# Kernel tuning notes

Hardware: AMD Instinct MI355X
Metric: run time of the kernel (lower is better)

Reference implementation:

```python
import jax, jax.numpy as jnp
import numpy as np
import math

NUM_HEADS = 8
RES_K = 9  # res_kernel_size


def setup_inputs() -> dict:
    key = jax.random.key(0)
    ks = jax.random.split(key, 6)
    N, C, h, w = 8, 256, 64, 64
    x = jax.random.normal(ks[0], (N, C, h, w), dtype=jnp.float32)
    w_qkv = jax.random.normal(ks[1], (3 * C, C), dtype=jnp.float32) * 0.02
    b_qkv = jax.random.normal(ks[2], (3 * C,), dtype=jnp.float32) * 0.02
    w_proj = jax.random.normal(ks[3], (C, C), dtype=jnp.float32) * 0.02
    b_proj = jax.random.normal(ks[4], (C,), dtype=jnp.float32) * 0.02
    w_dconv = jax.random.normal(ks[5], (NUM_HEADS, 1, RES_K, 1), dtype=jnp.float32) * 0.1
    return {"x": x, "w_qkv": w_qkv, "b_qkv": b_qkv,
            "w_proj": w_proj, "b_proj": b_proj, "w_dconv": w_dconv}


def _l2norm(t):
    # torch x / x.norm(dim=-1, keepdim=True): plain L2 norm, no eps
    return t / jnp.linalg.norm(t, axis=-1, keepdims=True)


def reference(x, w_qkv, b_qkv, w_proj, b_proj, w_dconv):
    N, C, h, w = x.shape
    H = NUM_HEADS
    D = C // H
    L = h * w
    xt = x.reshape(N, C, L).transpose(0, 2, 1)  # [N, L, C]
    qkv = xt @ w_qkv.T + b_qkv                   # [N, L, 3C]
    qkv = qkv.reshape(N, L, 3, H, D).transpose(2, 0, 3, 1, 4)  # [3, N, H, L, D]
    q, k, v = qkv[0], qkv[1], qkv[2]
    q = _l2norm(q)
    k = _l2norm(k)
    # depthwise conv over token dim: v as NCHW with C=H, H=L, W=D
    pad = RES_K // 2
    dconv_v = jax.lax.conv_general_dilated(
        v, w_dconv, window_strides=(1, 1), padding=[(pad, pad), (0, 0)],
        dimension_numbers=("NCHW", "OIHW", "NCHW"), feature_group_count=H)
    attn = jnp.einsum("nhld,nhle->nhde", k, v)   # [N, H, D, D]
    out = 0.5 * v + (1.0 / math.pi) * jnp.einsum("nhld,nhde->nhle", q, attn)
    out = _l2norm(out)
    out = out + dconv_v
    out = out.transpose(0, 2, 1, 3).reshape(N, L, C)  # [N, L, C]
    out = out @ w_proj.T + b_proj
    return out.transpose(0, 2, 1).reshape(N, C, h, w)
```

## Files before the change

kernel.cpp:

```cpp
#include <hip/hip_runtime.h>

#define NB 8
#define CC 256
#define HH 8
#define DD 32
#define LL 4096

typedef short v8s __attribute__((ext_vector_type(8)));
typedef float v4f __attribute__((ext_vector_type(4)));
typedef unsigned short v8u __attribute__((ext_vector_type(8)));
typedef unsigned short v4us __attribute__((ext_vector_type(4)));

__device__ __forceinline__ float4 ld4(const float* p) { return *(const float4*)p; }

__device__ __forceinline__ unsigned short f2bf(float f) {
    union { float f; unsigned int u; } v; v.f = f;
    unsigned int r = (v.u + 0x7FFFu + ((v.u >> 16) & 1u)) >> 16;
    return (unsigned short)r;
}
__device__ __forceinline__ float bf2f(unsigned short u) {
    union { unsigned int u; float f; } v; v.u = ((unsigned int)u) << 16;
    return v.f;
}

__device__ __forceinline__ void gl_lds16(const unsigned short* g, unsigned short* l) {
    __builtin_amdgcn_global_load_lds(
        (const __attribute__((address_space(1))) void*)g,
        (__attribute__((address_space(3))) void*)l, 16, 0, 0);
}

__global__ __launch_bounds__(256) void cvt2_k(
    const float* __restrict__ a, const float* __restrict__ b,
    unsigned short* __restrict__ da, unsigned short* __restrict__ db,
    float* __restrict__ attn)
{
    int i = blockIdx.x * 256 + threadIdx.x;
    if (i < 3 * CC * CC) da[i] = f2bf(a[i]);
    else if (i < 4 * CC * CC) db[i - 3 * CC * CC] = f2bf(b[i - 3 * CC * CC]);
    else attn[i - 4 * CC * CC] = 0.f;
}

#define PADC 264
__global__ __launch_bounds__(256) void transpose_x_k(
    const float* __restrict__ x, unsigned short* __restrict__ xb)
{
    __shared__ unsigned short t[32][PADC];
    const int n = blockIdx.y;
    const int l0 = blockIdx.x * 32;
    const float* xn = x + (size_t)n * CC * LL;
    const int lam = threadIdx.x & 31;
    const int cb = threadIdx.x >> 5;
#pragma unroll
    for (int i = 0; i < 32; ++i) {
        int c = cb * 32 + i;
        t[lam][c] = f2bf(xn[(size_t)c * LL + l0 + lam]);
    }
    __syncthreads();
    unsigned short* dst = xb + ((size_t)n * LL + l0) * CC;
    const int tid = threadIdx.x;
#pragma unroll
    for (int i = 0; i < 4; ++i) {
        int f = i * 2048 + tid * 8;
        int lr = f >> 8;
        int c2 = f & 255;
        v8u val = *(const v8u*)&t[lr][c2];
        *(v8u*)(dst + f) = val;
    }
}

__global__ __launch_bounds__(256, 2) void gemm_qkv_mfma(
    const unsigned short* __restrict__ xb, const unsigned short* __restrict__ wqb,
    const float* __restrict__ bqkv,
    unsigned short* __restrict__ q, unsigned short* __restrict__ k,
    unsigned short* __restrict__ v)
{
    __shared__ __align__(16) unsigned short xs[8192];
    __shared__ __align__(16) unsigned short wsb[16384];

    const int bid  = blockIdx.x;
    const int xcd  = bid & 7;
    const int slot = bid >> 3;
    const int jt   = slot % 3;
    const int p    = slot / 3;
    const int gp   = xcd * 32 + p;
    const int l0   = (gp & 31) * 128;
    const int n    = gp >> 5;
    const int j0   = jt * 256;

    const int tid = threadIdx.x;
    const int lane = tid & 63, wave = tid >> 6;
    const int wr = wave >> 1, wc = wave & 1;
    const int r = lane & 15, quad = lane >> 4;

    const int srow = wave * 8 + (lane >> 3);
    const int dchunk = (lane & 7) ^ (lane >> 3);
    const unsigned short* xg = xb + (size_t)n * LL * CC
                             + (size_t)(l0 + srow) * CC + dchunk * 8;
    const unsigned short* wg = wqb + (size_t)(j0 + srow) * CC + dchunk * 8;
    unsigned short* xls = xs + wave * 512 + lane * 8;
    unsigned short* wls = wsb + wave * 512 + lane * 8;

    v4f acc[8][4];
#pragma unroll
    for (int mi = 0; mi < 8; ++mi)
#pragma unroll
        for (int nj = 0; nj < 4; ++nj) acc[mi][nj] = (v4f)(0.f);

    const int jbase = wr * 128;
    const int lbase = wc * 64;

    for (int kt = 0; kt < 4; ++kt) {
        if (kt) __syncthreads();
        const int c0 = kt * 64;
#pragma unroll
        for (int i = 0; i < 4; ++i)
            gl_lds16(xg + (size_t)i * 32 * CC + c0, xls + i * 2048);
#pragma unroll
        for (int i = 0; i < 8; ++i)
            gl_lds16(wg + (size_t)i * 32 * CC + c0, wls + i * 2048);
        __syncthreads();

#pragma unroll
        for (int kk = 0; kk < 2; ++kk) {
            const int cfrag = kk * 4 + quad;
            const int s = cfrag ^ (r & 7);
            v8s b[4];
#pragma unroll
            for (int nj = 0; nj < 4; ++nj) {
                int lloc = lbase + nj * 16 + r;
                b[nj] = *(const v8s*)(xs + lloc * 64 + s * 8);
            }
            v8s a[8];
#pragma unroll
            for (int mi = 0; mi < 8; ++mi) {
                int jloc = jbase + mi * 16 + r;
                a[mi] = *(const v8s*)(wsb + jloc * 64 + s * 8);
            }
#pragma unroll
            for (int mi = 0; mi < 8; ++mi)
#pragma unroll
                for (int nj = 0; nj < 4; ++nj)
                    acc[mi][nj] = __builtin_amdgcn_mfma_f32_16x16x32_bf16(
                        a[mi], b[nj], acc[mi][nj], 0, 0, 0);
        }
    }

    unsigned short* base = (jt == 0 ? q : (jt == 1 ? k : v));

    float bias[8][4];
#pragma unroll
    for (int mi = 0; mi < 8; ++mi)
        *(float4*)bias[mi] = *(const float4*)(bqkv + j0 + jbase + mi * 16 + quad * 4);

    unsigned short* dstp[8];
#pragma unroll
    for (int mi = 0; mi < 8; ++mi) {
        int hh = wr * 4 + (mi >> 1);
        int d0 = (mi & 1) * 16 + quad * 4;
        dstp[mi] = base + (size_t)(n * HH + hh) * LL * DD + d0;
    }

    if (jt < 2) {
#pragma unroll
        for (int nj = 0; nj < 4; ++nj) {
            float t[8][4];
            float ss[4] = {0.f, 0.f, 0.f, 0.f};
#pragma unroll
            for (int mi = 0; mi < 8; ++mi)
#pragma unroll
                for (int reg = 0; reg < 4; ++reg) {
                    float val = acc[mi][nj][reg] + bias[mi][reg];
                    t[mi][reg] = val;
                    ss[mi >> 1] += val * val;
                }
#pragma unroll
            for (int h4 = 0; h4 < 4; ++h4) {
                ss[h4] += __shfl_xor(ss[h4], 16);
                ss[h4] += __shfl_xor(ss[h4], 32);
                ss[h4] = rsqrtf(ss[h4]);
            }
            size_t l = (size_t)(l0 + lbase + nj * 16 + r);
#pragma unroll
            for (int mi = 0; mi < 8; ++mi) {
                float rn = ss[mi >> 1];
                v4us pk;
#pragma unroll
                for (int reg = 0; reg < 4; ++reg) pk[reg] = f2bf(t[mi][reg] * rn);
                *(v4us*)(dstp[mi] + l * DD) = pk;
            }
        }
    } else {
#pragma unroll
        for (int nj = 0; nj < 4; ++nj) {
            size_t l = (size_t)(l0 + lbase + nj * 16 + r);
#pragma unroll
            for (int mi = 0; mi < 8; ++mi) {
                v4us pk;
#pragma unroll
                for (int reg = 0; reg < 4; ++reg)
                    pk[reg] = f2bf(acc[mi][nj][reg] + bias[mi][reg]);
                *(v4us*)(dstp[mi] + l * DD) = pk;
            }
        }
    }
}

__global__ __launch_bounds__(256) void attn_k(
    const unsigned short* __restrict__ k, const unsigned short* __restrict__ v,
    float* __restrict__ attn)
{
    __shared__ float red[4][1024];
    const int nh = blockIdx.y;
    const int wv = threadIdx.x >> 6;
    const int lane = threadIdx.x & 63;
    const int eg = lane & 7;
    const int dg = lane >> 3;
    const int l0 = blockIdx.x * 512 + wv * 128;
    const unsigned short* kb = k + (size_t)nh * LL * DD;
    const unsigned short* vb = v + (size_t)nh * LL * DD;
    float acc[4][4] = {};
#pragma unroll 4
    for (int l = l0; l < l0 + 128; ++l) {
        v4us k4 = *(const v4us*)(kb + (size_t)l * DD + dg * 4);
        v4us v4 = *(const v4us*)(vb + (size_t)l * DD + eg * 4);
        float ka[4] = {bf2f(k4[0]), bf2f(k4[1]), bf2f(k4[2]), bf2f(k4[3])};
        float va[4] = {bf2f(v4[0]), bf2f(v4[1]), bf2f(v4[2]), bf2f(v4[3])};
#pragma unroll
        for (int dp = 0; dp < 4; ++dp)
#pragma unroll
            for (int ep = 0; ep < 4; ++ep)
                acc[dp][ep] += ka[dp] * va[ep];
    }
#pragma unroll
    for (int dp = 0; dp < 4; ++dp)
#pragma unroll
        for (int ep = 0; ep < 4; ++ep)
            red[wv][(dg * 4 + dp) * 32 + eg * 4 + ep] = acc[dp][ep];
    __syncthreads();
    float* ap = attn + (size_t)nh * 1024;
    for (int i = threadIdx.x; i < 1024; i += 256)
        atomicAdd(&ap[i], red[0][i] + red[1][i] + red[2][i] + red[3][i]);
}

#define TOK 256
__global__ __launch_bounds__(256) void mid_k(
    const unsigned short* __restrict__ q, const unsigned short* __restrict__ v,
    const float* __restrict__ attn, const float* __restrict__ wd,
    unsigned short* __restrict__ midb)
{
    __shared__ float vt[TOK + 8][34];
    const int nh = blockIdx.y;
    const int n = nh >> 3, hh = nh & 7;
    const int l0 = blockIdx.x * TOK;
    const int tid = threadIdx.x;
    const int lane = tid & 63, wave = tid >> 6;
    const int r = lane & 15, quad = lane >> 4;
    const unsigned short* vb = v + (size_t)nh * LL * DD;

    for (int f = tid; f < (TOK + 8) * 4; f += 256) {
        int row = f >> 2, seg = f & 3;
        int l = l0 - 4 + row;
        float tmp[8];
        if (l >= 0 && l < LL) {
            v8u v8 = *(const v8u*)(vb + (size_t)l * DD + seg * 8);
#pragma unroll
            for (int j = 0; j < 8; ++j) tmp[j] = bf2f(v8[j]);
        } else {
#pragma unroll
            for (int j = 0; j < 8; ++j) tmp[j] = 0.f;
        }
#pragma unroll
        for (int j = 0; j < 8; ++j) vt[row][seg * 8 + j] = tmp[j];
    }

    v8s bfrag[2];
#pragma unroll
    for (int et = 0; et < 2; ++et) {
        int e = et * 16 + r;
#pragma unroll
        for (int j = 0; j < 8; ++j)
            ((unsigned short*)&bfrag[et])[j] =
                f2bf(attn[(size_t)nh * 1024 + (quad * 8 + j) * 32 + e]);
    }

    float wc[9];
#pragma unroll
    for (int r9 = 0; r9 < 9; ++r9) wc[r9] = wd[hh * 9 + r9];

    __syncthreads();

    const unsigned short* qb = q + (size_t)nh * LL * DD;
    unsigned short* ob = midb + (size_t)n * LL * CC + hh * DD;

#pragma unroll
    for (int tp = 0; tp < 4; ++tp) {
        const int tb = wave * 64 + tp * 16;
        v8s afrag = *(const v8s*)(qb + (size_t)(l0 + tb + r) * DD + quad * 8);
        v4f acc[2] = {(v4f)(0.f), (v4f)(0.f)};
#pragma unroll
        for (int et = 0; et < 2; ++et)
            acc[et] = __builtin_amdgcn_mfma_f32_16x16x32_bf16(afrag, bfrag[et], acc[et], 0, 0, 0);

        float vcol[2][12];
#pragma unroll
        for (int et = 0; et < 2; ++et) {
            int e = et * 16 + r;
#pragma unroll
            for (int o = 0; o < 12; ++o)
                vcol[et][o] = vt[tb + quad * 4 + o][e];
        }

        float t[2][4], ss[4];
#pragma unroll
        for (int reg = 0; reg < 4; ++reg) {
            t[0][reg] = 0.5f * vcol[0][4 + reg] + 0.31830988618379067f * acc[0][reg];
            t[1][reg] = 0.5f * vcol[1][4 + reg] + 0.31830988618379067f * acc[1][reg];
            ss[reg] = t[0][reg] * t[0][reg] + t[1][reg] * t[1][reg];
        }
#pragma unroll
        for (int m = 1; m < 16; m <<= 1)
#pragma unroll
            for (int reg = 0; reg < 4; ++reg)
                ss[reg] += __shfl_xor(ss[reg], m);
#pragma unroll
        for (int reg = 0; reg < 4; ++reg) ss[reg] = rsqrtf(ss[reg]);

#pragma unroll
        for (int et = 0; et < 2; ++et) {
            int e = et * 16 + r;
#pragma unroll
            for (int reg = 0; reg < 4; ++reg) {
                float dv = 0.f;
#pragma unroll
                for (int r9 = 0; r9 < 9; ++r9) dv += wc[r9] * vcol[et][reg + r9];
                int l = l0 + tb + quad * 4 + reg;
                ob[(size_t)l * CC + e] = f2bf(t[et][reg] * ss[reg] + dv);
            }
        }
    }
}

__global__ __launch_bounds__(256, 2) void gemm_proj_mfma(
    const unsigned short* __restrict__ midb, const unsigned short* __restrict__ wpb,
    const float* __restrict__ bp, float* __restrict__ out)
{
    __shared__ __align__(16) unsigned short xs[8192];
    __shared__ __align__(16) unsigned short wsb[8192];

    const int bid  = blockIdx.x;
    const int xcd  = bid & 7;
    const int slot = bid >> 3;
    const int jt   = slot & 1;
    const int p    = slot >> 1;
    const int gp   = xcd * 32 + p;
    const int l0   = (gp & 31) * 128;
    const int n    = gp >> 5;
    const int j0   = jt * 128;

    const int tid = threadIdx.x;
    const int lane = tid & 63, wave = tid >> 6;
    const int wr = wave >> 1, wc = wave & 1;
    const int r = lane & 15, quad = lane >> 4;

    const int srow = wave * 8 + (lane >> 3);
    const int dchunk = (lane & 7) ^ (lane >> 3);
    const unsigned short* xg = midb + (size_t)n * LL * CC
                             + (size_t)(l0 + srow) * CC + dchunk * 8;
    const unsigned short* wg = wpb + (size_t)(j0 + srow) * CC + dchunk * 8;
    unsigned short* xls = xs + wave * 512 + lane * 8;
    unsigned short* wls = wsb + wave * 512 + lane * 8;

    v4f acc[4][4];
#pragma unroll
    for (int mi = 0; mi < 4; ++mi)
#pragma unroll
        for (int nj = 0; nj < 4; ++nj) acc[mi][nj] = (v4f)(0.f);

    const int jbase = wr * 64;
    const int lbase = wc * 64;

    for (int kt = 0; kt < 4; ++kt) {
        if (kt) __syncthreads();
        const int c0 = kt * 64;
#pragma unroll
        for (int i = 0; i < 4; ++i) {
            gl_lds16(xg + (size_t)i * 32 * CC + c0, xls + i * 2048);
            gl_lds16(wg + (size_t)i * 32 * CC + c0, wls + i * 2048);
        }
        __syncthreads();

        v8s a[4][2], b[4][2];
#pragma unroll
        for (int kk = 0; kk < 2; ++kk) {
            const int cfrag = kk * 4 + quad;
#pragma unroll
            for (int mi = 0; mi < 4; ++mi) {
                int jloc = jbase + mi * 16 + r;
                int s = cfrag ^ (r & 7);
                a[mi][kk] = *(const v8s*)(wsb + jloc * 64 + s * 8);
            }
#pragma unroll
            for (int nj = 0; nj < 4; ++nj) {
                int lloc = lbase + nj * 16 + r;
                int s = cfrag ^ (r & 7);
                b[nj][kk] = *(const v8s*)(xs + lloc * 64 + s * 8);
            }
        }
#pragma unroll
        for (int kk = 0; kk < 2; ++kk)
#pragma unroll
            for (int mi = 0; mi < 4; ++mi)
#pragma unroll
                for (int nj = 0; nj < 4; ++nj)
                    acc[mi][nj] = __builtin_amdgcn_mfma_f32_16x16x32_bf16(
                        a[mi][kk], b[nj][kk], acc[mi][nj], 0, 0, 0);
    }

#pragma unroll
    for (int mi = 0; mi < 4; ++mi)
#pragma unroll
        for (int reg = 0; reg < 4; ++reg) {
            int j = j0 + jbase + mi * 16 + quad * 4 + reg;
            float bias = bp[j];
#pragma unroll
            for (int nj = 0; nj < 4; ++nj) {
                int l = l0 + lbase + nj * 16 + r;
                out[((size_t)n * CC + j) * LL + l] = acc[mi][nj][reg] + bias;
            }
        }
}

extern "C" void kernel_launch(void* const* d_in, const int* in_sizes, int n_in,
                              void* d_out, int out_size, void* d_ws, size_t ws_size,
                              hipStream_t stream)
{
    const float* x     = (const float*)d_in[0];
    const float* wqkv  = (const float*)d_in[1];
    const float* bqkv  = (const float*)d_in[2];
    const float* wproj = (const float*)d_in[3];
    const float* bproj = (const float*)d_in[4];
    const float* wd    = (const float*)d_in[5];
    float* out = (float*)d_out;

    const size_t QKV = (size_t)NB * HH * LL * DD;
    unsigned short* q = (unsigned short*)d_ws;
    unsigned short* k = q + QKV;
    unsigned short* v = k + QKV;
    float* attn = (float*)(v + QKV);
    unsigned short* xb = (unsigned short*)(attn + (size_t)NB * HH * DD * DD);
    unsigned short* midb = xb;
    unsigned short* wqb = xb + (size_t)NB * LL * CC;
    unsigned short* wpb = wqb + 3 * CC * CC;

    cvt2_k<<<1280, 256, 0, stream>>>(wqkv, wproj, wqb, wpb, attn);
    transpose_x_k<<<dim3(128, 8), 256, 0, stream>>>(x, xb);
    gemm_qkv_mfma<<<768, 256, 0, stream>>>(xb, wqb, bqkv, q, k, v);
    attn_k<<<dim3(8, 64), 256, 0, stream>>>(k, v, attn);
    mid_k<<<dim3(LL / TOK, 64), 256, 0, stream>>>(q, v, attn, wd, midb);
    gemm_proj_mfma<<<512, 256, 0, stream>>>(midb, wpb, bproj, out);
}
```

Before: 157.8 us.

## Fuse mid stage into projection GEMM and merge prep kernels

The per-head mid computation (q·attn, normalisation, depthwise conv) now writes its bf16 result into a swizzled shared-memory tile, and the same block runs the output projection GEMM on it. This avoids the round trip of the intermediate tensor through global memory and one kernel launch. The weight conversion, attn zeroing and x transpose are merged into a single vectorised prep kernel. In exchange, each block computes all 8 heads for 64 tokens and reads the projection weights directly from global memory/L2 without LDS staging, which may cost bandwidth and occupancy.

```diff
diff --git a/kernel.cpp b/kernel.cpp
--- a/kernel.cpp
+++ b/kernel.cpp
@@ -29,42 +29,57 @@
         (__attribute__((address_space(3))) void*)l, 16, 0, 0);
 }
 
-__global__ __launch_bounds__(256) void cvt2_k(
-    const float* __restrict__ a, const float* __restrict__ b,
-    unsigned short* __restrict__ da, unsigned short* __restrict__ db,
+#define PADC 264
+__global__ __launch_bounds__(256) void prep_k(
+    const float* __restrict__ x, unsigned short* __restrict__ xb,
+    const float* __restrict__ wq, const float* __restrict__ wp,
+    unsigned short* __restrict__ dwq, unsigned short* __restrict__ dwp,
     float* __restrict__ attn)
 {
-    int i = blockIdx.x * 256 + threadIdx.x;
-    if (i < 3 * CC * CC) da[i] = f2bf(a[i]);
-    else if (i < 4 * CC * CC) db[i - 3 * CC * CC] = f2bf(b[i - 3 * CC * CC]);
-    else attn[i - 4 * CC * CC] = 0.f;
-}
-
-#define PADC 264
-__global__ __launch_bounds__(256) void transpose_x_k(
-    const float* __restrict__ x, unsigned short* __restrict__ xb)
-{
     __shared__ unsigned short t[32][PADC];
-    const int n = blockIdx.y;
-    const int l0 = blockIdx.x * 32;
-    const float* xn = x + (size_t)n * CC * LL;
-    const int lam = threadIdx.x & 31;
-    const int cb = threadIdx.x >> 5;
-#pragma unroll
-    for (int i = 0; i < 32; ++i) {
-        int c = cb * 32 + i;
-        t[lam][c] = f2bf(xn[(size_t)c * LL + l0 + lam]);
-    }
-    __syncthreads();
-    unsigned short* dst = xb + ((size_t)n * LL + l0) * CC;
-    const int tid = threadIdx.x;
-#pragma unroll
-    for (int i = 0; i < 4; ++i) {
-        int f = i * 2048 + tid * 8;
-        int lr = f >> 8;
-        int c2 = f & 255;
-        v8u val = *(const v8u*)&t[lr][c2];
-        *(v8u*)(dst + f) = val;
+    const int bid = blockIdx.x;
+    if (bid < 1024) {
+        const int n = bid >> 7;
+        const int l0 = (bid & 127) * 32;
+        const float* xn = x + (size_t)n * CC * LL;
+        const int lam = threadIdx.x & 31;
+        const int cb = threadIdx.x >> 5;
+#pragma unroll
+        for (int i = 0; i < 32; ++i) {
+            int c = cb * 32 + i;
+            t[lam][c] = f2bf(xn[(size_t)c * LL + l0 + lam]);
+        }
+        __syncthreads();
+        unsigned short* dst = xb + ((size_t)n * LL + l0) * CC;
+        const int tid = threadIdx.x;
+#pragma unroll
+        for (int i = 0; i < 4; ++i) {
+            int f = i * 2048 + tid * 8;
+            int lr = f >> 8;
+            int c2 = f & 255;
+            v8u val = *(const v8u*)&t[lr][c2];
+            *(v8u*)(dst + f) = val;
+        }
+    } else {
+        int ti = (bid - 1024) * 256 + threadIdx.x;
+        if (ti < 24576) {
+            int i = ti * 8;
+            float4 f0 = ld4(wq + i), f1 = ld4(wq + i + 4);
+            v8u o;
+            o[0] = f2bf(f0.x); o[1] = f2bf(f0.y); o[2] = f2bf(f0.z); o[3] = f2bf(f0.w);
+            o[4] = f2bf(f1.x); o[5] = f2bf(f1.y); o[6] = f2bf(f1.z); o[7] = f2bf(f1.w);
+            *(v8u*)(dwq + i) = o;
+        } else if (ti < 32768) {
+            int i = (ti - 24576) * 8;
+            float4 f0 = ld4(wp + i), f1 = ld4(wp + i + 4);
+            v8u o;
+            o[0] = f2bf(f0.x); o[1] = f2bf(f0.y); o[2] = f2bf(f0.z); o[3] = f2bf(f0.w);
+            o[4] = f2bf(f1.x); o[5] = f2bf(f1.y); o[6] = f2bf(f1.z); o[7] = f2bf(f1.w);
+            *(v8u*)(dwp + i) = o;
+        } else {
+            int i = (ti - 32768) * 4;
+            *(float4*)(attn + i) = make_float4(0.f, 0.f, 0.f, 0.f);
+        }
     }
 }
 
@@ -242,168 +257,139 @@
         atomicAdd(&ap[i], red[0][i] + red[1][i] + red[2][i] + red[3][i]);
 }
 
-#define TOK 256
-__global__ __launch_bounds__(256) void mid_k(
+#define PTOK 64
+#define VTP 40
+__global__ __launch_bounds__(256, 2) void midproj_k(
     const unsigned short* __restrict__ q, const unsigned short* __restrict__ v,
     const float* __restrict__ attn, const float* __restrict__ wd,
-    unsigned short* __restrict__ midb)
+    const unsigned short* __restrict__ wpb, const float* __restrict__ bp,
+    float* __restrict__ out)
 {
-    __shared__ float vt[TOK + 8][34];
-    const int nh = blockIdx.y;
-    const int n = nh >> 3, hh = nh & 7;
-    const int l0 = blockIdx.x * TOK;
+    __shared__ __align__(16) unsigned short vt[8 * 72 * VTP];
+    __shared__ __align__(16) unsigned short smid[4 * 64 * 64];
+
+    const int n  = blockIdx.y;
+    const int l0 = blockIdx.x * PTOK;
     const int tid = threadIdx.x;
     const int lane = tid & 63, wave = tid >> 6;
     const int r = lane & 15, quad = lane >> 4;
-    const unsigned short* vb = v + (size_t)nh * LL * DD;
-
-    for (int f = tid; f < (TOK + 8) * 4; f += 256) {
-        int row = f >> 2, seg = f & 3;
+
+    const unsigned short* vbase = v + (size_t)(n * HH) * LL * DD;
+#pragma unroll
+    for (int it = 0; it < 9; ++it) {
+        int task = it * 256 + tid;
+        int seg = task & 3;
+        int hr = task >> 2;
+        int row = hr % 72;
+        int h = hr / 72;
         int l = l0 - 4 + row;
-        float tmp[8];
-        if (l >= 0 && l < LL) {
-            v8u v8 = *(const v8u*)(vb + (size_t)l * DD + seg * 8);
-#pragma unroll
-            for (int j = 0; j < 8; ++j) tmp[j] = bf2f(v8[j]);
-        } else {
-#pragma unroll
-            for (int j = 0; j < 8; ++j) tmp[j] = 0.f;
-        }
-#pragma unroll
-        for (int j = 0; j < 8; ++j) vt[row][seg * 8 + j] = tmp[j];
-    }
-
-    v8s bfrag[2];
-#pragma unroll
-    for (int et = 0; et < 2; ++et) {
-        int e = et * 16 + r;
-#pragma unroll
-        for (int j = 0; j < 8; ++j)
-            ((unsigned short*)&bfrag[et])[j] =
-                f2bf(attn[(size_t)nh * 1024 + (quad * 8 + j) * 32 + e]);
-    }
-
-    float wc[9];
-#pragma unroll
-    for (int r9 = 0; r9 < 9; ++r9) wc[r9] = wd[hh * 9 + r9];
-
+        v8u val;
+        if (l >= 0 && l < LL)
+            val = *(const v8u*)(vbase + ((size_t)h * LL + l) * DD + seg * 8);
+        else
+            val = (v8u)(unsigned short)0;
+        *(v8u*)(&vt[hr * VTP + seg * 8]) = val;
+    }
     __syncthreads();
 
-    const unsigned short* qb = q + (size_t)nh * LL * DD;
-    unsigned short* ob = midb + (size_t)n * LL * CC + hh * DD;
-
-#pragma unroll
-    for (int tp = 0; tp < 4; ++tp) {
-        const int tb = wave * 64 + tp * 16;
-        v8s afrag = *(const v8s*)(qb + (size_t)(l0 + tb + r) * DD + quad * 8);
-        v4f acc[2] = {(v4f)(0.f), (v4f)(0.f)};
-#pragma unroll
-        for (int et = 0; et < 2; ++et)
-            acc[et] = __builtin_amdgcn_mfma_f32_16x16x32_bf16(afrag, bfrag[et], acc[et], 0, 0, 0);
-
-        float vcol[2][12];
+    const float inv_pi = 0.31830988618379067f;
+#pragma unroll
+    for (int hi = 0; hi < 2; ++hi) {
+        const int h = wave * 2 + hi;
+        const int nh = n * HH + h;
+        const unsigned short* qb = q + (size_t)nh * LL * DD;
+        const unsigned short* vth = vt + h * 72 * VTP;
+
+        v8s bfrag[2];
 #pragma unroll
         for (int et = 0; et < 2; ++et) {
             int e = et * 16 + r;
 #pragma unroll
-            for (int o = 0; o < 12; ++o)
-                vcol[et][o] = vt[tb + quad * 4 + o][e];
-        }
-
-        float t[2][4], ss[4];
-#pragma unroll
-        for (int reg = 0; reg < 4; ++reg) {
-            t[0][reg] = 0.5f * vcol[0][4 + reg] + 0.31830988618379067f * acc[0][reg];
-            t[1][reg] = 0.5f * vcol[1][4 + reg] + 0.31830988618379067f * acc[1][reg];
-            ss[reg] = t[0][reg] * t[0][reg] + t[1][reg] * t[1][reg];
-        }
-#pragma unroll
-        for (int m = 1; m < 16; m <<= 1)
-#pragma unroll
-            for (int reg = 0; reg < 4; ++reg)
-                ss[reg] += __shfl_xor(ss[reg], m);
-#pragma unroll
-        for (int reg = 0; reg < 4; ++reg) ss[reg] = rsqrtf(ss[reg]);
-
-#pragma unroll
-        for (int et = 0; et < 2; ++et) {
-            int e = et * 16 + r;
+            for (int j = 0; j < 8; ++j)
+                ((unsigned short*)&bfrag[et])[j] =
+                    f2bf(attn[(size_t)nh * 1024 + (quad * 8 + j) * 32 + e]);
+        }
+        float wc[9];
+#pragma unroll
+        for (int r9 = 0; r9 < 9; ++r9) wc[r9] = wd[h * 9 + r9];
+
+#pragma unroll
+        for (int lt = 0; lt < 4; ++lt) {
+            const int tb = lt * 16;
+            v8s afrag = *(const v8s*)(qb + (size_t)(l0 + tb + r) * DD + quad * 8);
+            v4f acc[2] = {(v4f)(0.f), (v4f)(0.f)};
+#pragma unroll
+            for (int et = 0; et < 2; ++et)
+                acc[et] = __builtin_amdgcn_mfma_f32_16x16x32_bf16(
+                    afrag, bfrag[et], acc[et], 0, 0, 0);
+
+            float vcol[2][12];
+#pragma unroll
+            for (int et = 0; et < 2; ++et) {
+                int e = et * 16 + r;
+#pragma unroll
+                for (int o = 0; o < 12; ++o)
+                    vcol[et][o] = bf2f(vth[(tb + quad * 4 + o) * VTP + e]);
+            }
+
+            float t[2][4], ss[4];
 #pragma unroll
             for (int reg = 0; reg < 4; ++reg) {
-                float dv = 0.f;
-#pragma unroll
-                for (int r9 = 0; r9 < 9; ++r9) dv += wc[r9] * vcol[et][reg + r9];
-                int l = l0 + tb + quad * 4 + reg;
-                ob[(size_t)l * CC + e] = f2bf(t[et][reg] * ss[reg] + dv);
-            }
-        }
-    }
-}
-
-__global__ __launch_bounds__(256, 2) void gemm_proj_mfma(
-    const unsigned short* __restrict__ midb, const unsigned short* __restrict__ wpb,
-    const float* __restrict__ bp, float* __restrict__ out)
-{
-    __shared__ __align__(16) unsigned short xs[8192];
-    __shared__ __align__(16) unsigned short wsb[8192];
-
-    const int bid  = blockIdx.x;
-    const int xcd  = bid & 7;
-    const int slot = bid >> 3;
-    const int jt   = slot & 1;
-    const int p    = slot >> 1;
-    const int gp   = xcd * 32 + p;
-    const int l0   = (gp & 31) * 128;
-    const int n    = gp >> 5;
-    const int j0   = jt * 128;
-
-    const int tid = threadIdx.x;
-    const int lane = tid & 63, wave = tid >> 6;
-    const int wr = wave >> 1, wc = wave & 1;
-    const int r = lane & 15, quad = lane >> 4;
-
-    const int srow = wave * 8 + (lane >> 3);
-    const int dchunk = (lane & 7) ^ (lane >> 3);
-    const unsigned short* xg = midb + (size_t)n * LL * CC
-                             + (size_t)(l0 + srow) * CC + dchunk * 8;
-    const unsigned short* wg = wpb + (size_t)(j0 + srow) * CC + dchunk * 8;
-    unsigned short* xls = xs + wave * 512 + lane * 8;
-    unsigned short* wls = wsb + wave * 512 + lane * 8;
-
+                t[0][reg] = 0.5f * vcol[0][4 + reg] + inv_pi * acc[0][reg];
+                t[1][reg] = 0.5f * vcol[1][4 + reg] + inv_pi * acc[1][reg];
+                ss[reg] = t[0][reg] * t[0][reg] + t[1][reg] * t[1][reg];
+            }
+#pragma unroll
+            for (int m = 1; m < 16; m <<= 1)
+#pragma unroll
+                for (int reg = 0; reg < 4; ++reg)
+                    ss[reg] += __shfl_xor(ss[reg], m);
+#pragma unroll
+            for (int reg = 0; reg < 4; ++reg) ss[reg] = rsqrtf(ss[reg]);
+
+#pragma unroll
+            for (int et = 0; et < 2; ++et) {
+                int c = h * 32 + et * 16 + r;
+                int chunk = c >> 6, c6 = c & 63;
+                int goff = c6 & 7;
+#pragma unroll
+                for (int reg = 0; reg < 4; ++reg) {
+                    float dv = 0.f;
+#pragma unroll
+                    for (int r9 = 0; r9 < 9; ++r9) dv += wc[r9] * vcol[et][reg + r9];
+                    int l = tb + quad * 4 + reg;
+                    int g = (c6 >> 3) ^ (l & 7);
+                    smid[chunk * 4096 + l * 64 + g * 8 + goff] =
+                        f2bf(t[et][reg] * ss[reg] + dv);
+                }
+            }
+        }
+    }
+    __syncthreads();
+
+    const int jbase = wave * 64;
     v4f acc[4][4];
 #pragma unroll
     for (int mi = 0; mi < 4; ++mi)
 #pragma unroll
         for (int nj = 0; nj < 4; ++nj) acc[mi][nj] = (v4f)(0.f);
 
-    const int jbase = wr * 64;
-    const int lbase = wc * 64;
-
+#pragma unroll
     for (int kt = 0; kt < 4; ++kt) {
-        if (kt) __syncthreads();
-        const int c0 = kt * 64;
-#pragma unroll
-        for (int i = 0; i < 4; ++i) {
-            gl_lds16(xg + (size_t)i * 32 * CC + c0, xls + i * 2048);
-            gl_lds16(wg + (size_t)i * 32 * CC + c0, wls + i * 2048);
-        }
-        __syncthreads();
-
         v8s a[4][2], b[4][2];
 #pragma unroll
         for (int kk = 0; kk < 2; ++kk) {
             const int cfrag = kk * 4 + quad;
 #pragma unroll
             for (int mi = 0; mi < 4; ++mi) {
-                int jloc = jbase + mi * 16 + r;
-                int s = cfrag ^ (r & 7);
-                a[mi][kk] = *(const v8s*)(wsb + jloc * 64 + s * 8);
-            }
+                int j = jbase + mi * 16 + r;
+                a[mi][kk] = *(const v8s*)(wpb + (size_t)j * CC + kt * 64 + cfrag * 8);
+            }
+            const int s = cfrag ^ (r & 7);
 #pragma unroll
             for (int nj = 0; nj < 4; ++nj) {
-                int lloc = lbase + nj * 16 + r;
-                int s = cfrag ^ (r & 7);
-                b[nj][kk] = *(const v8s*)(xs + lloc * 64 + s * 8);
+                int lloc = nj * 16 + r;
+                b[nj][kk] = *(const v8s*)(smid + kt * 4096 + lloc * 64 + s * 8);
             }
         }
 #pragma unroll
@@ -420,11 +406,11 @@
     for (int mi = 0; mi < 4; ++mi)
 #pragma unroll
         for (int reg = 0; reg < 4; ++reg) {
-            int j = j0 + jbase + mi * 16 + quad * 4 + reg;
+            int j = jbase + mi * 16 + quad * 4 + reg;
             float bias = bp[j];
 #pragma unroll
             for (int nj = 0; nj < 4; ++nj) {
-                int l = l0 + lbase + nj * 16 + r;
+                int l = l0 + nj * 16 + r;
                 out[((size_t)n * CC + j) * LL + l] = acc[mi][nj][reg] + bias;
             }
         }
@@ -448,14 +434,11 @@
     unsigned short* v = k + QKV;
     float* attn = (float*)(v + QKV);
     unsigned short* xb = (unsigned short*)(attn + (size_t)NB * HH * DD * DD);
-    unsigned short* midb = xb;
     unsigned short* wqb = xb + (size_t)NB * LL * CC;
     unsigned short* wpb = wqb + 3 * CC * CC;
 
-    cvt2_k<<<1280, 256, 0, stream>>>(wqkv, wproj, wqb, wpb, attn);
-    transpose_x_k<<<dim3(128, 8), 256, 0, stream>>>(x, xb);
+    prep_k<<<1216, 256, 0, stream>>>(x, xb, wqkv, wproj, wqb, wpb, attn);
     gemm_qkv_mfma<<<768, 256, 0, stream>>>(xb, wqb, bqkv, q, k, v);
     attn_k<<<dim3(8, 64), 256, 0, stream>>>(k, v, attn);
-    mid_k<<<dim3(LL / TOK, 64), 256, 0, stream>>>(q, v, attn, wd, midb);
-    gemm_proj_mfma<<<512, 256, 0, stream>>>(midb, wpb, bproj, out);
-}
+    midproj_k<<<dim3(LL / PTOK, NB), 256, 0, stream>>>(q, v, attn, wd, wpb, bproj, out);
+}
```

New measurement: 155.7 us. About the same (-1.3%).
